# Kernel optimization log

Measured on AMD Instinct MI355X. Metric: run time of the kernel, lower is better.

Reference implementation:

```python
import jax, jax.numpy as jnp
import numpy as np
import math

MODEL_DIM = 4096
NUM_EXPERTS = 64
NUM_TOKENS = 8192
CAPACITY_FACTOR = 1.0
MIN_CAPACITY = 4


def setup_inputs() -> dict:
    key = jax.random.key(0)
    k1, k2, k3 = jax.random.split(key, 3)
    x = jax.random.normal(k1, (NUM_TOKENS, MODEL_DIM), dtype=jnp.float32)
    wg_weight = jax.random.normal(k2, (NUM_EXPERTS, MODEL_DIM), dtype=jnp.float32) * (1.0 / math.sqrt(MODEL_DIM))
    uniform_noise = jax.random.uniform(k3, (NUM_TOKENS, NUM_EXPERTS), dtype=jnp.float32)
    return {"x": x, "wg_weight": wg_weight, "uniform_noise": uniform_noise}


def reference(x, wg_weight, uniform_noise):
    # gate projection in fp32 (torch module forces .float())
    logits = jnp.einsum('sd,ed->se', x.astype(jnp.float32), wg_weight.astype(jnp.float32))
    gates = jax.nn.softmax(logits, axis=1)  # [s, e]
    s, e = gates.shape
    capacity = max(math.ceil(s / e * CAPACITY_FACTOR), MIN_CAPACITY)  # static: 128

    indices1_s = jnp.argmax(gates, axis=1)                      # [s]
    mask1 = jax.nn.one_hot(indices1_s, e, dtype=jnp.int32)      # [s, e]
    exp_counts = jnp.sum(mask1, axis=0)                         # [e]

    # load-balancing aux loss
    me = jnp.mean(gates, axis=0)
    ce = jnp.mean(mask1.astype(jnp.float32), axis=0)
    l_aux = jnp.sum(me * ce) * e

    # random capacity selection: per-expert top-`capacity` tokens by uniform noise
    mask1_rand = mask1.astype(jnp.float32) * uniform_noise      # [s, e]
    _, top_idx = jax.lax.top_k(mask1_rand.T, capacity)          # [e, capacity] token ids
    sel = jnp.zeros((s, e), jnp.int32).at[top_idx, jnp.arange(e)[:, None]].set(1)
    new_mask1 = mask1 * sel                                     # [s, e]

    # capacity-slot assignment via cumsum
    locations1 = jnp.cumsum(new_mask1, axis=0) - 1              # [s, e]
    locations1_s = jnp.sum(locations1 * new_mask1, axis=1)      # [s]

    gates_masked = gates * new_mask1.astype(jnp.float32)        # [s, e]
    locations1_sc = jax.nn.one_hot(locations1_s, capacity, dtype=jnp.float32)  # [s, c]
    combine_weights = jnp.einsum('se,sc->sec', gates_masked, locations1_sc)     # [s, e, c]
    dispatch_mask = combine_weights.astype(bool)
    return l_aux, combine_weights, dispatch_mask, exp_counts
```

## Files before the change

### kernel.cpp

```cpp
#include <hip/hip_runtime.h>

#define S    8192
#define Dm   4096
#define E    64
#define CAP  128
#define CCH  32
#define KC   (Dm/CCH)
#define TBv  512
#define KSUB 32
#define XSTR 33

#define CW_OFF 1
#define DM_OFF (1 + (size_t)S*E*CAP)
#define EC_OFF (1 + 2*(size_t)S*E*CAP)

__global__ void k0_transpose(const float* __restrict__ wg, float* __restrict__ wt2) {
    const int e  = blockIdx.x >> 2;
    const int kb = (blockIdx.x & 3) * 1024;
    const int t  = threadIdx.x;
    const float4 v = *(const float4*)(wg + (size_t)e * Dm + kb + t * 4);
    wt2[(size_t)(kb + t*4 + 0) * E + e] = v.x;
    wt2[(size_t)(kb + t*4 + 1) * E + e] = v.y;
    wt2[(size_t)(kb + t*4 + 2) * E + e] = v.z;
    wt2[(size_t)(kb + t*4 + 3) * E + e] = v.w;
}

__global__ __launch_bounds__(256, 2)
void k1_partial(const float* __restrict__ x, const float* __restrict__ wt2,
                float* __restrict__ part) {
    __shared__ float  xs[TBv * XSTR];
    __shared__ float4 ws4[KSUB * 16];
    const int tb  = blockIdx.x >> 5;
    const int c   = blockIdx.x & 31;
    const int tid = threadIdx.x;
    const int lane = tid & 63;
    const int wv   = tid >> 6;
    const int k0 = c * KC;

    const int ta = wv * 128 + lane;
    const int xa_base = ta * XSTR;
    const int xb_base = xa_base + 64 * XSTR;

    float acca[64], accb[64];
    #pragma unroll
    for (int e = 0; e < 64; e++) { acca[e] = 0.f; accb[e] = 0.f; }

    const int r0 = tid >> 3;
    const int c4 = tid & 7;

    for (int su = 0; su < KC / KSUB; su++) {
        const int ks0 = k0 + su * KSUB;
        #pragma unroll
        for (int i = 0; i < 16; i++) {
            const int row = i * 32 + r0;
            const float4 v = *(const float4*)(x + (size_t)(tb*TBv + row) * Dm + ks0 + c4*4);
            float* p = xs + row * XSTR + c4 * 4;
            p[0] = v.x; p[1] = v.y; p[2] = v.z; p[3] = v.w;
        }
        {
            const float* wsrc = wt2 + (size_t)ks0 * E;
            ws4[tid]       = *(const float4*)(wsrc + tid * 4);
            ws4[tid + 256] = *(const float4*)(wsrc + 1024 + tid * 4);
        }
        __syncthreads();
        #pragma unroll 2
        for (int kk = 0; kk < KSUB; kk++) {
            const float xa = xs[xa_base + kk];
            const float xb = xs[xb_base + kk];
            #pragma unroll
            for (int e4 = 0; e4 < 16; e4++) {
                const float4 w = ws4[kk * 16 + e4];
                acca[e4*4+0] = fmaf(xa, w.x, acca[e4*4+0]);
                acca[e4*4+1] = fmaf(xa, w.y, acca[e4*4+1]);
                acca[e4*4+2] = fmaf(xa, w.z, acca[e4*4+2]);
                acca[e4*4+3] = fmaf(xa, w.w, acca[e4*4+3]);
                accb[e4*4+0] = fmaf(xb, w.x, accb[e4*4+0]);
                accb[e4*4+1] = fmaf(xb, w.y, accb[e4*4+1]);
                accb[e4*4+2] = fmaf(xb, w.z, accb[e4*4+2]);
                accb[e4*4+3] = fmaf(xb, w.w, accb[e4*4+3]);
            }
        }
        __syncthreads();
    }
    const size_t tok_a = (size_t)tb * TBv + ta;
    float* pa = part + ((size_t)c * S + tok_a) * E;
    float* pb = pa + 64 * E;
    #pragma unroll
    for (int e4 = 0; e4 < 16; e4++) {
        *(float4*)(pa + e4*4) = make_float4(acca[e4*4], acca[e4*4+1], acca[e4*4+2], acca[e4*4+3]);
        *(float4*)(pb + e4*4) = make_float4(accb[e4*4], accb[e4*4+1], accb[e4*4+2], accb[e4*4+3]);
    }
}

__global__ __launch_bounds__(256, 1)
void k1b_softmax(const float* __restrict__ part, float* __restrict__ gate_val,
                 int* __restrict__ idx1, int* __restrict__ counts,
                 float* __restrict__ me_sum) {
    const int tid = threadIdx.x, wv = tid >> 6, ln = tid & 63;
    const int token = blockIdx.x * 4 + wv;
    float p = 0.f;
    #pragma unroll
    for (int c = 0; c < CCH; c++) p += part[((size_t)c * S + token) * E + ln];
    float v = p; int i = ln;
    #pragma unroll
    for (int off = 1; off < 64; off <<= 1) {
        float ov = __shfl_xor(v, off, 64);
        int   oi = __shfl_xor(i, off, 64);
        if (ov > v || (ov == v && oi < i)) { v = ov; i = oi; }
    }
    float g = __expf(p - v);
    float ssum = g;
    #pragma unroll
    for (int off = 1; off < 64; off <<= 1) ssum += __shfl_xor(ssum, off, 64);
    const float gate = g / ssum;
    __shared__ float gs[4][64];
    gs[wv][ln] = gate;
    __syncthreads();
    if (tid < 64)
        atomicAdd(&me_sum[tid], gs[0][tid] + gs[1][tid] + gs[2][tid] + gs[3][tid]);
    if (ln == 0) {
        gate_val[token] = 1.0f / ssum;
        idx1[token] = i;
        atomicAdd(&counts[i], 1);
    }
}

__device__ __forceinline__ int block_reduce_sum(int v, int* tmp4, int tid) {
    #pragma unroll
    for (int off = 1; off < 64; off <<= 1) v += __shfl_xor(v, off, 64);
    __syncthreads();
    if ((tid & 63) == 0) tmp4[tid >> 6] = v;
    __syncthreads();
    return tmp4[0] + tmp4[1] + tmp4[2] + tmp4[3];
}

__device__ __forceinline__ int block_scan_incl(int val, int* a, int* b, int tid, int* total) {
    __syncthreads();
    a[tid] = val;
    __syncthreads();
    int* src = a; int* dst = b;
    #pragma unroll
    for (int off = 1; off < 256; off <<= 1) {
        int v = src[tid];
        if (tid >= off) v += src[tid - off];
        dst[tid] = v;
        __syncthreads();
        int* t = src; src = dst; dst = t;
    }
    *total = src[255];
    return src[tid];
}

__global__ __launch_bounds__(256, 1)
void k2_select(const int* __restrict__ idx1, const float* __restrict__ gate_val,
               const float* __restrict__ noise, const int* __restrict__ counts,
               const float* __restrict__ me_sum, float* __restrict__ out) {
    const int e = blockIdx.x;
    const int tid = threadIdx.x;
    __shared__ int idx_s[S];
    __shared__ unsigned short l_tok[S];
    __shared__ float l_ns[S];
    __shared__ int sa[256], sb[256];
    __shared__ int tmp4[4];

    for (int i = tid; i < S; i += 256) idx_s[i] = idx1[i];
    __syncthreads();

    int cnt = 0;
    #pragma unroll
    for (int j4 = 0; j4 < 8; j4++) {
        const int4 q = *(const int4*)&idx_s[tid * 32 + j4 * 4];
        cnt += (q.x == e) + (q.y == e) + (q.z == e) + (q.w == e);
    }
    int total_n;
    int incl = block_scan_incl(cnt, sa, sb, tid, &total_n);
    int pos = incl - cnt;
    const int n = total_n;
    #pragma unroll
    for (int j4 = 0; j4 < 8; j4++) {
        const int4 q = *(const int4*)&idx_s[tid * 32 + j4 * 4];
        const int qv[4] = {q.x, q.y, q.z, q.w};
        #pragma unroll
        for (int u = 0; u < 4; u++) {
            const int s = tid * 32 + j4 * 4 + u;
            if (qv[u] == e) {
                l_tok[pos] = (unsigned short)s;
                l_ns[pos]  = noise[(size_t)s * E + e];
                pos++;
            }
        }
    }
    __syncthreads();

    if (tid == 0) out[EC_OFF + e] = (float)n;

    unsigned int V = 0u;
    if (n > CAP) {
        unsigned int lo = 0u, hi = 0x3F800000u;
        while (hi - lo > 1u) {
            const unsigned int mid = (lo + hi) >> 1;
            int c = 0;
            for (int i2 = tid; i2 < n; i2 += 256)
                c += (__float_as_uint(l_ns[i2]) >= mid);
            const int cge = block_reduce_sum(c, tmp4, tid);
            if (cge >= CAP) lo = mid; else hi = mid;
        }
        V = lo;
    }

    const int m = (n + 255) >> 8;
    const int i_begin = min(n, tid * m);
    const int i_end   = min(n, i_begin + m);
    int gt_l = 0, eq_l = 0;
    for (int i2 = i_begin; i2 < i_end; i2++) {
        const unsigned int b = __float_as_uint(l_ns[i2]);
        gt_l += (b > V); eq_l += (b == V);
    }
    int tot_gt, tot_eq;
    const int incl_gt = block_scan_incl(gt_l, sa, sb, tid, &tot_gt);
    (void)incl_gt;
    const int incl_eq = block_scan_incl(eq_l, sa, sb, tid, &tot_eq);
    const int eq_excl = incl_eq - eq_l;
    const int take_eq = CAP - tot_gt;
    const int sel_l = gt_l + max(0, min(eq_l, take_eq - eq_excl));
    int tot_sel;
    const int incl_sel = block_scan_incl(sel_l, sa, sb, tid, &tot_sel);
    int slot = incl_sel - sel_l;
    int eq_seen = eq_excl;
    for (int i2 = i_begin; i2 < i_end; i2++) {
        const unsigned int b = __float_as_uint(l_ns[i2]);
        bool sel;
        if (b > V) sel = true;
        else if (b == V) { sel = (eq_seen < take_eq); eq_seen++; }
        else sel = false;
        if (sel) {
            const int tok = l_tok[i2];
            const float g = gate_val[tok];
            const size_t off = (size_t)tok * (E * CAP) + (size_t)e * CAP + slot;
            out[CW_OFF + off] = g;
            out[DM_OFF + off] = 1.0f;
            slot++;
        }
    }

    if (e == 0 && tid < 64) {
        float la = (me_sum[tid] / (float)S) * ((float)counts[tid] / (float)S);
        #pragma unroll
        for (int off = 1; off < 64; off <<= 1) la += __shfl_xor(la, off, 64);
        if (tid == 0) out[0] = la * (float)E;
    }
}

extern "C" void kernel_launch(void* const* d_in, const int* in_sizes, int n_in,
                              void* d_out, int out_size, void* d_ws, size_t ws_size,
                              hipStream_t stream) {
    const float* x     = (const float*)d_in[0];
    const float* wg    = (const float*)d_in[1];
    const float* noise = (const float*)d_in[2];
    float* out = (float*)d_out;
    float* ws  = (float*)d_ws;

    float* gate_val = ws;
    int*   idx1     = (int*)(ws + 8192);
    int*   counts   = (int*)(ws + 16384);
    float* me_sum   = ws + 16448;
    float* wt2      = ws + 16512;
    float* part     = ws + 16512 + 262144;

    hipMemsetAsync(counts, 0, 128 * sizeof(int), stream);
    hipMemsetAsync(out, 0, (size_t)out_size * sizeof(float), stream);
    k0_transpose<<<dim3(256),  dim3(256), 0, stream>>>(wg, wt2);
    k1_partial  <<<dim3(512),  dim3(256), 0, stream>>>(x, wt2, part);
    k1b_softmax <<<dim3(S/4),  dim3(256), 0, stream>>>(part, gate_val, idx1, counts, me_sum);
    k2_select   <<<dim3(E),    dim3(256), 0, stream>>>(idx1, gate_val, noise, counts, me_sum, out);
}
```

Baseline: 798.9 us.

## Retile gate GEMM to 4x16 register blocks with transposed x tile in LDS

Changes the gate projection kernel from each thread owning two tokens across all 64 experts to each thread owning 4 tokens by 16 experts, with x stored k-major in shared memory so threads read float4 token vectors. Block token tile shrinks from 512 to 256 and the K split from 32 to 16 chunks, which halves the partial-sum buffer traffic. The intent is better register reuse per LDS load and a smaller shared footprint. The cost is more blocks per K chunk, longer K loops per block, and bank-conflict-prone transposed LDS stores.

Result: faster. 719.9 us (-9.9%).

```diff
diff --git a/kernel.cpp b/kernel.cpp
--- a/kernel.cpp
+++ b/kernel.cpp
@@ -4,11 +4,10 @@
 #define Dm   4096
 #define E    64
 #define CAP  128
-#define CCH  32
+#define CCH  16
 #define KC   (Dm/CCH)
-#define TBv  512
 #define KSUB 32
-#define XSTR 33
+#define XSTR 260
 
 #define CW_OFF 1
 #define DM_OFF (1 + (size_t)S*E*CAP)
@@ -28,67 +27,64 @@
 __global__ __launch_bounds__(256, 2)
 void k1_partial(const float* __restrict__ x, const float* __restrict__ wt2,
                 float* __restrict__ part) {
-    __shared__ float  xs[TBv * XSTR];
+    __shared__ float  xs[KSUB * XSTR];
     __shared__ float4 ws4[KSUB * 16];
-    const int tb  = blockIdx.x >> 5;
-    const int c   = blockIdx.x & 31;
+    const int tb  = blockIdx.x >> 4;
+    const int c   = blockIdx.x & 15;
     const int tid = threadIdx.x;
-    const int lane = tid & 63;
-    const int wv   = tid >> 6;
-    const int k0 = c * KC;
-
-    const int ta = wv * 128 + lane;
-    const int xa_base = ta * XSTR;
-    const int xb_base = xa_base + 64 * XSTR;
-
-    float acca[64], accb[64];
-    #pragma unroll
-    for (int e = 0; e < 64; e++) { acca[e] = 0.f; accb[e] = 0.f; }
-
-    const int r0 = tid >> 3;
-    const int c4 = tid & 7;
+    const int tg  = tid & 63;
+    const int ng  = tid >> 6;
+    const int k0  = c * KC;
+
+    float acc[64];
+    #pragma unroll
+    for (int i = 0; i < 64; i++) acc[i] = 0.f;
+
+    const int c4   = tid & 7;
+    const int trow = tid >> 3;
 
     for (int su = 0; su < KC / KSUB; su++) {
         const int ks0 = k0 + su * KSUB;
         #pragma unroll
-        for (int i = 0; i < 16; i++) {
-            const int row = i * 32 + r0;
-            const float4 v = *(const float4*)(x + (size_t)(tb*TBv + row) * Dm + ks0 + c4*4);
-            float* p = xs + row * XSTR + c4 * 4;
-            p[0] = v.x; p[1] = v.y; p[2] = v.z; p[3] = v.w;
+        for (int i = 0; i < 8; i++) {
+            const int token = i * 32 + trow;
+            const float4 v = *(const float4*)(x + (size_t)(tb*256 + token) * Dm + ks0 + c4*4);
+            xs[(c4*4+0)*XSTR + token] = v.x;
+            xs[(c4*4+1)*XSTR + token] = v.y;
+            xs[(c4*4+2)*XSTR + token] = v.z;
+            xs[(c4*4+3)*XSTR + token] = v.w;
         }
         {
-            const float* wsrc = wt2 + (size_t)ks0 * E;
-            ws4[tid]       = *(const float4*)(wsrc + tid * 4);
-            ws4[tid + 256] = *(const float4*)(wsrc + 1024 + tid * 4);
+            const float4* wsrc = (const float4*)(wt2 + (size_t)ks0 * E);
+            ws4[tid]       = wsrc[tid];
+            ws4[tid + 256] = wsrc[tid + 256];
         }
         __syncthreads();
         #pragma unroll 2
         for (int kk = 0; kk < KSUB; kk++) {
-            const float xa = xs[xa_base + kk];
-            const float xb = xs[xb_base + kk];
+            const float4 a = *(const float4*)&xs[kk * XSTR + tg * 4];
+            const float av[4] = {a.x, a.y, a.z, a.w};
             #pragma unroll
-            for (int e4 = 0; e4 < 16; e4++) {
-                const float4 w = ws4[kk * 16 + e4];
-                acca[e4*4+0] = fmaf(xa, w.x, acca[e4*4+0]);
-                acca[e4*4+1] = fmaf(xa, w.y, acca[e4*4+1]);
-                acca[e4*4+2] = fmaf(xa, w.z, acca[e4*4+2]);
-                acca[e4*4+3] = fmaf(xa, w.w, acca[e4*4+3]);
-                accb[e4*4+0] = fmaf(xb, w.x, accb[e4*4+0]);
-                accb[e4*4+1] = fmaf(xb, w.y, accb[e4*4+1]);
-                accb[e4*4+2] = fmaf(xb, w.z, accb[e4*4+2]);
-                accb[e4*4+3] = fmaf(xb, w.w, accb[e4*4+3]);
+            for (int q = 0; q < 4; q++) {
+                const float4 w = ws4[kk * 16 + ng * 4 + q];
+                #pragma unroll
+                for (int j = 0; j < 4; j++) {
+                    acc[j*16 + q*4+0] = fmaf(av[j], w.x, acc[j*16 + q*4+0]);
+                    acc[j*16 + q*4+1] = fmaf(av[j], w.y, acc[j*16 + q*4+1]);
+                    acc[j*16 + q*4+2] = fmaf(av[j], w.z, acc[j*16 + q*4+2]);
+                    acc[j*16 + q*4+3] = fmaf(av[j], w.w, acc[j*16 + q*4+3]);
+                }
             }
         }
         __syncthreads();
     }
-    const size_t tok_a = (size_t)tb * TBv + ta;
-    float* pa = part + ((size_t)c * S + tok_a) * E;
-    float* pb = pa + 64 * E;
-    #pragma unroll
-    for (int e4 = 0; e4 < 16; e4++) {
-        *(float4*)(pa + e4*4) = make_float4(acca[e4*4], acca[e4*4+1], acca[e4*4+2], acca[e4*4+3]);
-        *(float4*)(pb + e4*4) = make_float4(accb[e4*4], accb[e4*4+1], accb[e4*4+2], accb[e4*4+3]);
+    #pragma unroll
+    for (int j = 0; j < 4; j++) {
+        float* dst = part + ((size_t)c * S + tb*256 + tg*4 + j) * E + ng*16;
+        #pragma unroll
+        for (int q = 0; q < 4; q++)
+            *(float4*)(dst + q*4) = make_float4(acc[j*16+q*4+0], acc[j*16+q*4+1],
+                                                acc[j*16+q*4+2], acc[j*16+q*4+3]);
     }
 }
 
```
